# Kernel tuning notes

Hardware: AMD Instinct MI355X
Metric: run time of the kernel (lower is better)

Reference implementation:

```python
import jax, jax.numpy as jnp
import numpy as np
import math

B, S, D = 4, 2048, 1024
H = 16
DH = D // H
NEG = -1e20


def setup_inputs() -> dict:
    key = jax.random.key(0)
    ks = jax.random.split(key, 8)
    Q_batch = jax.random.normal(ks[0], (B, S, D), dtype=jnp.float32)
    K_batch = jax.random.normal(ks[1], (B, S, D), dtype=jnp.float32)
    V_batch = jax.random.normal(ks[2], (B, S, D), dtype=jnp.float32)
    valid_lens = jax.random.randint(ks[3], (B,), 0, S).astype(jnp.int64)
    # LazyLinear weights, stored as (in, out) so projection is x @ W
    sc = 1.0 / math.sqrt(D)
    Wq = jax.random.normal(ks[4], (D, D), dtype=jnp.float32) * sc
    Wk = jax.random.normal(ks[5], (D, D), dtype=jnp.float32) * sc
    Wv = jax.random.normal(ks[6], (D, D), dtype=jnp.float32) * sc
    Wo = jax.random.normal(ks[7], (D, D), dtype=jnp.float32) * sc
    return {"Q_batch": Q_batch, "K_batch": K_batch, "V_batch": V_batch,
            "valid_lens": valid_lens, "Wq": Wq, "Wk": Wk, "Wv": Wv, "Wo": Wo}


def reference(Q_batch, K_batch, V_batch, valid_lens, Wq, Wk, Wv, Wo):
    b, nq, _ = Q_batch.shape
    nk = K_batch.shape[1]
    # project and split heads (feature dim split head-major, matching transpose_qkv)
    q = (Q_batch @ Wq).reshape(b, nq, H, DH).transpose(0, 2, 1, 3)  # (b,h,nq,dh)
    k = (K_batch @ Wk).reshape(b, nk, H, DH).transpose(0, 2, 1, 3)  # (b,h,nk,dh)
    v = (V_batch @ Wv).reshape(b, nk, H, DH).transpose(0, 2, 1, 3)  # (b,h,nk,dh)
    scores = jnp.einsum('bhqd,bhkd->bhqk', q, k) / math.sqrt(DH)
    # mask keys at position >= valid_lens[b] (shared across heads and queries)
    key_pos = jnp.arange(nk)
    mask = key_pos[None, None, None, :] < valid_lens[:, None, None, None]
    scores = jnp.where(mask, scores, NEG)
    w = jax.nn.softmax(scores, axis=-1)  # dropout rate 0 -> identity
    o = jnp.einsum('bhqk,bhkd->bhqd', w, v)           # (b,h,nq,dh)
    o = o.transpose(0, 2, 1, 3).reshape(b, nq, H * DH)  # concat heads
    return o @ Wo
```

## Files before the change

kernel.cpp:

```cpp
#include <hip/hip_runtime.h>
#include <stdint.h>

typedef unsigned short u16;
using bf16x8 = __attribute__((ext_vector_type(8))) __bf16;
using f32x4  = __attribute__((ext_vector_type(4))) float;
using u16x8  = __attribute__((ext_vector_type(8))) unsigned short;
using u16x4  = __attribute__((ext_vector_type(4))) unsigned short;

#define NH   16
#define DHD  64
#define SEQ  2048
#define DD   1024

__device__ inline u16 bfbits(float f) {
    __bf16 h = (__bf16)f;
    return __builtin_bit_cast(u16, h);
}

__device__ inline void gld16(const u16* g, u16* l) {
    __builtin_amdgcn_global_load_lds(
        (const __attribute__((address_space(1))) void*)g,
        (__attribute__((address_space(3))) void*)l,
        16, 0, 0);
}

__global__ __launch_bounds__(256) void transpose4(
    const float* __restrict__ s0, const float* __restrict__ s1,
    const float* __restrict__ s2, const float* __restrict__ s3,
    u16* __restrict__ d0, u16* __restrict__ d1,
    u16* __restrict__ d2, u16* __restrict__ d3)
{
    const float* src = s0; u16* dst = d0;
    if (blockIdx.z == 1) { src = s1; dst = d1; }
    else if (blockIdx.z == 2) { src = s2; dst = d2; }
    else if (blockIdx.z == 3) { src = s3; dst = d3; }

    __shared__ u16 tile[32][33];
    int tx = threadIdx.x, ty = threadIdx.y;
    int x = blockIdx.x * 32 + tx;
    int y0 = blockIdx.y * 32 + ty;
#pragma unroll
    for (int i = 0; i < 32; i += 8)
        tile[ty + i][tx] = bfbits(src[(size_t)(y0 + i) * DD + x]);
    __syncthreads();
    int x2 = blockIdx.y * 32 + tx;
    int y2 = blockIdx.x * 32 + ty;
#pragma unroll
    for (int i = 0; i < 32; i += 8)
        dst[(size_t)(y2 + i) * DD + x2] = tile[tx][ty + i];
}

__global__ __launch_bounds__(256) void cvt3(
    const float* __restrict__ s0, const float* __restrict__ s1,
    const float* __restrict__ s2,
    u16* __restrict__ d0, u16* __restrict__ d1, u16* __restrict__ d2,
    const int* __restrict__ vl)
{
    const float* src = s0; u16* dst = d0;
    if (blockIdx.z == 1) { src = s1; dst = d1; }
    else if (blockIdx.z == 2) { src = s2; dst = d2; }

    if (blockIdx.z != 0) {
        int r = blockIdx.x * 2;
        int v = vl[r >> 11];
        int ve = (v == 0) ? SEQ : v;
        int lim = ((ve + 127) >> 7) << 7;
        if ((r & (SEQ - 1)) >= lim) return;
    }

    size_t i = ((size_t)blockIdx.x * 256 + threadIdx.x) * 8;
    f32x4 a = *(const f32x4*)&src[i];
    f32x4 b = *(const f32x4*)&src[i + 4];
    u16x8 o;
#pragma unroll
    for (int j = 0; j < 4; ++j) { o[j] = bfbits(a[j]); o[j + 4] = bfbits(b[j]); }
    *(u16x8*)&dst[i] = o;
}

__global__ __launch_bounds__(256) void cvt1(
    const float* __restrict__ src, u16* __restrict__ dst)
{
    size_t i = ((size_t)blockIdx.x * 256 + threadIdx.x) * 8;
    f32x4 a = *(const f32x4*)&src[i];
    f32x4 b = *(const f32x4*)&src[i + 4];
    u16x8 o;
#pragma unroll
    for (int j = 0; j < 4; ++j) { o[j] = bfbits(a[j]); o[j + 4] = bfbits(b[j]); }
    *(u16x8*)&dst[i] = o;
}

template<int MODE>
__global__ __launch_bounds__(256) void gemm_bt16(
    const u16* __restrict__ A0, const u16* __restrict__ A1, const u16* __restrict__ A2,
    const u16* __restrict__ B0, const u16* __restrict__ B1, const u16* __restrict__ B2,
    void* __restrict__ C0, void* __restrict__ C1, void* __restrict__ C2,
    const int* __restrict__ vl)
{
    const int K = 1024;
    const u16* A = A0; const u16* Bt = B0; void* C = C0;
    if (MODE == 3) {
        if (blockIdx.z == 1) { A = A1; Bt = B1; C = C1; }
        else if (blockIdx.z == 2) { A = A2; Bt = B2; C = C2; }
    }

    __shared__ __align__(16) u16 As[2][128 * 32];
    __shared__ __align__(16) u16 Bs[2][128 * 32];

    const int t = threadIdx.x;
    const int wave = t >> 6, lane = t & 63;
    const int l15 = lane & 15, q4 = lane >> 4;
    const int wm = (wave >> 1) * 64, wn = (wave & 1) * 64;

    const int gx = gridDim.x;
    const int nwg = gx * gridDim.y;
    int flat = blockIdx.y * gx + blockIdx.x;
    flat = (flat & 7) * (nwg >> 3) + (flat >> 3);
    const int m0 = (flat / gx) * 128, n0 = (flat % gx) * 128;

    if (MODE == 3 && blockIdx.z != 0) {
        int v = vl[m0 >> 11];
        int ve = (v == 0) ? SEQ : v;
        if ((m0 & (SEQ - 1)) >= ve) return;
    }

    const int ar = t >> 2;
    const int ac = (t & 3) * 8;

    const u16* gA = &A [(size_t)(m0 + ar) * K + ac];
    const u16* gB = &Bt[(size_t)(n0 + ar) * K + ac];
    u16* lA0 = &As[0][t * 8];
    u16* lA1 = &As[1][t * 8];
    u16* lB0 = &Bs[0][t * 8];
    u16* lB1 = &Bs[1][t * 8];

    f32x4 acc[4][4] = {};

    for (int k0 = 0; k0 < K; k0 += 64) {
        __syncthreads();
        gld16(gA + k0,                   lA0);
        gld16(gA + (size_t)64 * K + k0,  lA0 + 64 * 32);
        gld16(gA + k0 + 32,              lA1);
        gld16(gA + (size_t)64 * K + k0 + 32, lA1 + 64 * 32);
        gld16(gB + k0,                   lB0);
        gld16(gB + (size_t)64 * K + k0,  lB0 + 64 * 32);
        gld16(gB + k0 + 32,              lB1);
        gld16(gB + (size_t)64 * K + k0 + 32, lB1 + 64 * 32);
        __syncthreads();

#pragma unroll
        for (int hf = 0; hf < 2; ++hf) {
            bf16x8 af[4], bfr[4];
#pragma unroll
            for (int i = 0; i < 4; ++i) {
                af[i]  = *(const bf16x8*)&As[hf][(wm + i * 16 + l15) * 32 + q4 * 8];
                bfr[i] = *(const bf16x8*)&Bs[hf][(wn + i * 16 + l15) * 32 + q4 * 8];
            }
#pragma unroll
            for (int i = 0; i < 4; ++i)
#pragma unroll
                for (int j = 0; j < 4; ++j)
                    acc[i][j] = __builtin_amdgcn_mfma_f32_16x16x32_bf16(af[i], bfr[j], acc[i][j], 0, 0, 0);
        }
    }

    const bool vt_store = (MODE == 2) || (MODE == 3 && blockIdx.z == 2);

#pragma unroll
    for (int i = 0; i < 4; ++i) {
        int row_l = wm + i * 16 + q4 * 4;
#pragma unroll
        for (int j = 0; j < 4; ++j) {
            int col = n0 + wn + j * 16 + l15;
            if (MODE == 1) {
#pragma unroll
                for (int r = 0; r < 4; ++r) {
                    int row = m0 + row_l + r;
                    ((float*)C)[(size_t)row * DD + col] = acc[i][j][r];
                }
            } else if (vt_store) {
                int row = m0 + row_l;
                int b = row >> 11, s = row & (SEQ - 1);
                int h = col >> 6, dh = col & (DHD - 1);
                u16x4 pk;
#pragma unroll
                for (int r = 0; r < 4; ++r) pk[r] = bfbits(acc[i][j][r]);
                *(u16x4*)&((u16*)C)[(((size_t)(b * NH + h) * DHD + dh) << 11) | s] = pk;
            } else {
#pragma unroll
                for (int r = 0; r < 4; ++r) {
                    int row = m0 + row_l + r;
                    int b = row >> 11, s = row & (SEQ - 1);
                    int h = col >> 6, dh = col & (DHD - 1);
                    ((u16*)C)[(((size_t)(b * NH + h) * SEQ + s) << 6) | dh] = bfbits(acc[i][j][r]);
                }
            }
        }
    }
}

__global__ __launch_bounds__(256, 4) void attn(
    const u16* __restrict__ q_ws, const u16* __restrict__ k_ws,
    const u16* __restrict__ vT_ws, const int* __restrict__ valid_lens,
    u16* __restrict__ o_ws)
{
    const int bh = blockIdx.y;
    const int b = bh >> 4, h = bh & 15;
    const int qt = blockIdx.x;
    const int valid = valid_lens[b];
    const bool valid0 = (valid == 0);
    const int valid_eff = valid0 ? SEQ : valid;
    const int kt_n = (valid_eff + 63) >> 6;
    const float c2 = valid0 ? 0.f : 0.18033688011112042f;
    const float M2 = 17.312340490667562f;

    __shared__ __align__(16) u16 Kbuf[2][64 * 64];
    __shared__ __align__(16) u16 Vbuf[64 * 64];
    __shared__ __align__(16) u16 Ps[4][32][64];

    const int t = threadIdx.x;
    const int wave = t >> 6, lane = t & 63;
    const int l15 = lane & 15, q4 = lane >> 4;

    const size_t base  = (size_t)bh * SEQ * DHD;
    const size_t vbase = (size_t)bh * DHD * SEQ;

    const int q0 = qt * 128 + wave * 32;

    const int sr0 = wave * 16 + (lane >> 3);
    const int cg  = ((lane & 7) ^ (sr0 & 7)) * 8;
    const u16* gK = &k_ws [base  + (size_t)sr0 * DHD + cg];
    const u16* gV = &vT_ws[vbase + (size_t)sr0 * SEQ + cg];
    const int ldst = sr0 * 64 + (lane & 7) * 8;

    u16x8 ou;
#pragma unroll
    for (int j = 0; j < 8; ++j) ou[j] = 0x3F80;
    const bf16x8 ones = __builtin_bit_cast(bf16x8, ou);

    bf16x8 qf[2][2];
#pragma unroll
    for (int mi = 0; mi < 2; ++mi)
#pragma unroll
        for (int c = 0; c < 2; ++c)
            qf[mi][c] = *(const bf16x8*)&q_ws[base + (size_t)(q0 + mi * 16 + l15) * DHD + c * 32 + q4 * 8];

    f32x4 o4[2][4] = {};
    f32x4 l_acc[2] = {};

    const int swz  = (l15 & 7) * 8;

    gld16(gK,       &Kbuf[0][ldst]);
    gld16(gK + 512, &Kbuf[0][ldst + 512]);

    int cur = 0;
    for (int kt = 0; kt < kt_n; ++kt) {
        __syncthreads();
        {
            const u16* vv = gV + (size_t)kt * 64;
            gld16(vv,                   &Vbuf[ldst]);
            gld16(vv + (size_t)8 * SEQ, &Vbuf[ldst + 512]);
        }
        const bool pre = (kt + 1 < kt_n);
        if (pre) {
            const u16* kk = gK + (size_t)(kt + 1) * 64 * DHD;
            int bf = cur ^ 1;
            gld16(kk,       &Kbuf[bf][ldst]);
            gld16(kk + 512, &Kbuf[bf][ldst + 512]);
        }

        const u16* KK = Kbuf[cur];

        f32x4 s4[2][4] = {};
#pragma unroll
        for (int c = 0; c < 2; ++c)
#pragma unroll
            for (int ni = 0; ni < 4; ++ni) {
                bf16x8 kf = *(const bf16x8*)&KK[(ni * 16 + l15) * 64 + ((c * 32 + q4 * 8) ^ swz)];
#pragma unroll
                for (int mi = 0; mi < 2; ++mi)
                    s4[mi][ni] = __builtin_amdgcn_mfma_f32_16x16x32_bf16(kf, qf[mi][c], s4[mi][ni], 0, 0, 0);
            }

        const bool tile_full = valid0 || (kt * 64 + 64 <= valid_eff);
        if (tile_full) {
#pragma unroll
            for (int mi = 0; mi < 2; ++mi) {
                int qrow = mi * 16 + l15;
                int psw  = (l15 & 7) * 8;
#pragma unroll
                for (int ni = 0; ni < 4; ++ni) {
                    u16x4 pk;
#pragma unroll
                    for (int r = 0; r < 4; ++r) {
                        float p = __builtin_amdgcn_exp2f(__builtin_fmaf(s4[mi][ni][r], c2, -M2));
                        pk[r] = bfbits(p);
                    }
                    *(u16x4*)&Ps[wave][qrow][(ni * 16 + q4 * 4) ^ psw] = pk;
                }
            }
        } else {
#pragma unroll
            for (int mi = 0; mi < 2; ++mi) {
                int qrow = mi * 16 + l15;
                int psw  = (l15 & 7) * 8;
#pragma unroll
                for (int ni = 0; ni < 4; ++ni) {
                    u16x4 pk;
#pragma unroll
                    for (int r = 0; r < 4; ++r) {
                        bool ok = (kt * 64 + ni * 16 + q4 * 4 + r) < valid_eff;
                        float arg = ok ? __builtin_fmaf(s4[mi][ni][r], c2, -M2) : -1e30f;
                        pk[r] = bfbits(__builtin_amdgcn_exp2f(arg));
                    }
                    *(u16x4*)&Ps[wave][qrow][(ni * 16 + q4 * 4) ^ psw] = pk;
                }
            }
        }

        if (pre) asm volatile("s_waitcnt vmcnt(2)\n\ts_barrier" ::: "memory");
        else     asm volatile("s_waitcnt vmcnt(0)\n\ts_barrier" ::: "memory");

#pragma unroll
        for (int c = 0; c < 2; ++c) {
            bf16x8 pf[2];
#pragma unroll
            for (int mi = 0; mi < 2; ++mi) {
                pf[mi] = *(const bf16x8*)&Ps[wave][mi * 16 + l15][(c * 32 + q4 * 8) ^ ((l15 & 7) * 8)];
                l_acc[mi] = __builtin_amdgcn_mfma_f32_16x16x32_bf16(pf[mi], ones, l_acc[mi], 0, 0, 0);
            }
#pragma unroll
            for (int dt = 0; dt < 4; ++dt) {
                bf16x8 vf = *(const bf16x8*)&Vbuf[(dt * 16 + l15) * 64 + ((c * 32 + q4 * 8) ^ swz)];
#pragma unroll
                for (int mi = 0; mi < 2; ++mi)
                    o4[mi][dt] = __builtin_amdgcn_mfma_f32_16x16x32_bf16(pf[mi], vf, o4[mi][dt], 0, 0, 0);
            }
        }
        cur ^= 1;
    }

#pragma unroll
    for (int mi = 0; mi < 2; ++mi) {
        float inv[4];
#pragma unroll
        for (int r = 0; r < 4; ++r) inv[r] = 1.0f / l_acc[mi][r];
        int qrow = q0 + mi * 16 + q4 * 4;
#pragma unroll
        for (int dt = 0; dt < 4; ++dt) {
            int dh = dt * 16 + l15;
#pragma unroll
            for (int r = 0; r < 4; ++r) {
                float v = o4[mi][dt][r] * inv[r];
                o_ws[((size_t)(b * SEQ + qrow + r) << 10) | (h * DHD + dh)] = bfbits(v);
            }
        }
    }
}

extern "C" void kernel_launch(void* const* d_in, const int* in_sizes, int n_in,
                              void* d_out, int out_size, void* d_ws, size_t ws_size,
                              hipStream_t stream)
{
    (void)in_sizes; (void)n_in; (void)out_size;
    const float* Q  = (const float*)d_in[0];
    const float* Kb = (const float*)d_in[1];
    const float* V  = (const float*)d_in[2];
    const int*   vl = (const int*)d_in[3];
    const float* Wq = (const float*)d_in[4];
    const float* Wk = (const float*)d_in[5];
    const float* Wv = (const float*)d_in[6];
    const float* Wo = (const float*)d_in[7];
    float* out = (float*)d_out;

    char* ws = (char*)d_ws;
    u16* WqT   = (u16*)(ws + (size_t)0);
    u16* WkT   = (u16*)(ws + ((size_t)2 << 20));
    u16* WvT   = (u16*)(ws + ((size_t)4 << 20));
    u16* WoT   = (u16*)(ws + ((size_t)6 << 20));
    u16* q_ws  = (u16*)(ws + ((size_t)8 << 20));
    u16* k_ws  = (u16*)(ws + ((size_t)24 << 20));
    u16* vT_ws = (u16*)(ws + ((size_t)40 << 20));
    u16* o_ws  = (u16*)(ws + ((size_t)56 << 20));
    u16* Qbf   = (u16*)(ws + ((size_t)72 << 20));
    u16* Kbf   = (u16*)(ws + ((size_t)88 << 20));
    u16* Vbf   = (u16*)(ws + ((size_t)104 << 20));

    transpose4<<<dim3(32, 32, 4), dim3(32, 8), 0, stream>>>(
        Wq, Wk, Wv, Wo, WqT, WkT, WvT, WoT);

    const bool fused = ws_size >= ((size_t)120 << 20);
    if (fused) {
        cvt3<<<dim3(4096, 1, 3), 256, 0, stream>>>(Q, Kb, V, Qbf, Kbf, Vbf, vl);
        gemm_bt16<3><<<dim3(8, 64, 3), 256, 0, stream>>>(
            Qbf, Kbf, Vbf, WqT, WkT, WvT, q_ws, k_ws, vT_ws, vl);
    } else {
        cvt1<<<4096, 256, 0, stream>>>(Q, o_ws);
        gemm_bt16<0><<<dim3(8, 64), 256, 0, stream>>>(
            o_ws, nullptr, nullptr, WqT, nullptr, nullptr, q_ws, nullptr, nullptr, nullptr);
        cvt1<<<4096, 256, 0, stream>>>(Kb, o_ws);
        gemm_bt16<0><<<dim3(8, 64), 256, 0, stream>>>(
            o_ws, nullptr, nullptr, WkT, nullptr, nullptr, k_ws, nullptr, nullptr, nullptr);
        cvt1<<<4096, 256, 0, stream>>>(V, o_ws);
        gemm_bt16<2><<<dim3(8, 64), 256, 0, stream>>>(
            o_ws, nullptr, nullptr, WvT, nullptr, nullptr, vT_ws, nullptr, nullptr, nullptr);
    }

    attn<<<dim3(16, 64), 256, 0, stream>>>(q_ws, k_ws, vT_ws, vl, o_ws);

    gemm_bt16<1><<<dim3(8, 64), 256, 0, stream>>>(
        o_ws, nullptr, nullptr, WoT, nullptr, nullptr, out, nullptr, nullptr, nullptr);
}
```

Measured before the change: 289.8 us.

## Double-buffer GEMM k-tiles with prefetch and XOR-swizzled LDS layout

The bf16 projection GEMM now loads full 64-wide k-tiles into two LDS buffers. It issues the global-to-LDS copies for the next tile before computing on the current one, which drops the second barrier per iteration and lets memory latency overlap with MFMA work. The LDS tile uses 64-element rows with an XOR swizzle on 16-byte chunks to avoid bank conflicts on the fragment reads. In exchange, LDS use per block doubles, which may lower occupancy.

```diff
diff --git a/kernel.cpp b/kernel.cpp
--- a/kernel.cpp
+++ b/kernel.cpp
@@ -103,8 +103,8 @@
         else if (blockIdx.z == 2) { A = A2; Bt = B2; C = C2; }
     }
 
-    __shared__ __align__(16) u16 As[2][128 * 32];
-    __shared__ __align__(16) u16 Bs[2][128 * 32];
+    __shared__ __align__(16) u16 As[2][128 * 64];
+    __shared__ __align__(16) u16 Bs[2][128 * 64];
 
     const int t = threadIdx.x;
     const int wave = t >> 6, lane = t & 63;
@@ -123,37 +123,41 @@
         if ((m0 & (SEQ - 1)) >= ve) return;
     }
 
-    const int ar = t >> 2;
-    const int ac = (t & 3) * 8;
-
-    const u16* gA = &A [(size_t)(m0 + ar) * K + ac];
-    const u16* gB = &Bt[(size_t)(n0 + ar) * K + ac];
-    u16* lA0 = &As[0][t * 8];
-    u16* lA1 = &As[1][t * 8];
-    u16* lB0 = &Bs[0][t * 8];
-    u16* lB1 = &Bs[1][t * 8];
+    const int sr = t >> 3;
+    const int sg = (t & 7) ^ (sr & 7);
+    const u16* gA = &A [(size_t)(m0 + sr) * K + sg * 8];
+    const u16* gB = &Bt[(size_t)(n0 + sr) * K + sg * 8];
+
+    const int xr = (l15 & 7) * 8;
 
     f32x4 acc[4][4] = {};
 
+#pragma unroll
+    for (int is = 0; is < 4; ++is) {
+        gld16(gA + (size_t)(is * 32) * K, &As[0][is * 2048 + t * 8]);
+        gld16(gB + (size_t)(is * 32) * K, &Bs[0][is * 2048 + t * 8]);
+    }
+
+    int cur = 0;
     for (int k0 = 0; k0 < K; k0 += 64) {
         __syncthreads();
-        gld16(gA + k0,                   lA0);
-        gld16(gA + (size_t)64 * K + k0,  lA0 + 64 * 32);
-        gld16(gA + k0 + 32,              lA1);
-        gld16(gA + (size_t)64 * K + k0 + 32, lA1 + 64 * 32);
-        gld16(gB + k0,                   lB0);
-        gld16(gB + (size_t)64 * K + k0,  lB0 + 64 * 32);
-        gld16(gB + k0 + 32,              lB1);
-        gld16(gB + (size_t)64 * K + k0 + 32, lB1 + 64 * 32);
-        __syncthreads();
+        if (k0 + 64 < K) {
+            const int nb = cur ^ 1;
+            const size_t ko = k0 + 64;
+#pragma unroll
+            for (int is = 0; is < 4; ++is) {
+                gld16(gA + (size_t)(is * 32) * K + ko, &As[nb][is * 2048 + t * 8]);
+                gld16(gB + (size_t)(is * 32) * K + ko, &Bs[nb][is * 2048 + t * 8]);
+            }
+        }
 
 #pragma unroll
         for (int hf = 0; hf < 2; ++hf) {
             bf16x8 af[4], bfr[4];
 #pragma unroll
             for (int i = 0; i < 4; ++i) {
-                af[i]  = *(const bf16x8*)&As[hf][(wm + i * 16 + l15) * 32 + q4 * 8];
-                bfr[i] = *(const bf16x8*)&Bs[hf][(wn + i * 16 + l15) * 32 + q4 * 8];
+                af[i]  = *(const bf16x8*)&As[cur][(wm + i * 16 + l15) * 64 + ((hf * 32 + q4 * 8) ^ xr)];
+                bfr[i] = *(const bf16x8*)&Bs[cur][(wn + i * 16 + l15) * 64 + ((hf * 32 + q4 * 8) ^ xr)];
             }
 #pragma unroll
             for (int i = 0; i < 4; ++i)
@@ -161,6 +165,7 @@
                 for (int j = 0; j < 4; ++j)
                     acc[i][j] = __builtin_amdgcn_mfma_f32_16x16x32_bf16(af[i], bfr[j], acc[i][j], 0, 0, 0);
         }
+        cur ^= 1;
     }
 
     const bool vt_store = (MODE == 2) || (MODE == 3 && blockIdx.z == 2);
```

Result: faster. 279.5 us (-3.6%).
